# Kernel tuning notes

Hardware: AMD Instinct MI355X
Metric: run time of the kernel (lower is better)

## Reference

```python
import jax, jax.numpy as jnp
import numpy as np

NEG = -1e9
LRELU_ALPHA = 0.2  # tf.nn.leaky_relu default


def setup_inputs() -> dict:
    key = jax.random.key(0)
    k = jax.random.split(key, 6)
    B, N, F_in, F_out = 1, 8192, 256, 64
    x = jax.random.normal(k[0], (B, N, F_in), dtype=jnp.float32)
    # sparse adjacency as additive bias: ~32 neighbors/node on average
    u = jax.random.uniform(k[1], (B, N, N), dtype=jnp.float32)
    adj = jnp.where(u < 32.0 / N, 0.0, NEG).astype(jnp.float32)
    W = jax.random.normal(k[2], (F_in, F_out), dtype=jnp.float32) * (1.0 / np.sqrt(F_in))
    a1 = jax.random.normal(k[3], (F_out, 1), dtype=jnp.float32) * (1.0 / np.sqrt(F_out))
    a2 = jax.random.normal(k[4], (F_out, 1), dtype=jnp.float32) * (1.0 / np.sqrt(F_out))
    b1 = jnp.zeros((1,), dtype=jnp.float32)
    b2 = jnp.zeros((1,), dtype=jnp.float32)
    bias = jnp.zeros((F_out,), dtype=jnp.float32)
    return {"x": x, "adj": adj, "W": W, "a1": a1, "b1": b1, "a2": a2, "b2": b2, "bias": bias}


def reference(x, adj, W, a1, b1, a2, b2, bias):
    # conv1 (kernel_size=1, no bias) == per-node linear projection
    fts = jnp.einsum('bnf,fo->bno', x, W)            # [B, N, F_out]
    f1 = jnp.einsum('bno,oi->bni', fts, a1) + b1     # [B, N, 1]
    f2 = jnp.einsum('bno,oi->bni', fts, a2) + b2     # [B, N, 1]
    logits = f1 + jnp.swapaxes(f2, 1, 2)             # [B, N, N] additive scores
    scores = jax.nn.leaky_relu(logits, LRELU_ALPHA) + adj
    coefs = jax.nn.softmax(scores, axis=-1)          # [B, N, N]
    vals = jnp.einsum('bnm,bmo->bno', coefs, fts) + bias
    return jax.nn.elu(vals)
```

## Files before the change

kernel.cpp:

```cpp
#include <hip/hip_runtime.h>
#include <cstdint>

#define N_NODES 8192
#define F_IN    256
#define F_OUT   64
#define ALPHA   0.2f
#define CAPG    128

typedef float f32x4 __attribute__((ext_vector_type(4)));

__global__ __launch_bounds__(256) void k_proj(const float* __restrict__ x,
                                              const float* __restrict__ W,
                                              const float* __restrict__ a1,
                                              const float* __restrict__ b1,
                                              const float* __restrict__ a2,
                                              const float* __restrict__ b2,
                                              float* __restrict__ fts,
                                              float* __restrict__ f1,
                                              float* __restrict__ f2) {
    __shared__ __align__(16) float ws[64][F_OUT];
    const int t = threadIdx.x, lane = t & 63, w = t >> 6;
    const int rowA = blockIdx.x * 8 + w * 2;
    const int rowB = rowA + 1;

    const float4* xqA = (const float4*)(x + (size_t)rowA * F_IN);
    const float4* xqB = (const float4*)(x + (size_t)rowB * F_IN);
    float accA = 0.f, accB = 0.f;

    for (int kc = 0; kc < 4; ++kc) {
        if (kc) __syncthreads();
        {
            const float4* Wt = (const float4*)(W + (size_t)kc * 64 * F_OUT);
            float4* S = (float4*)&ws[0][0];
            S[t]       = Wt[t];
            S[t + 256] = Wt[t + 256];
            S[t + 512] = Wt[t + 512];
            S[t + 768] = Wt[t + 768];
        }
        __syncthreads();
        #pragma unroll
        for (int q = 0; q < 16; ++q) {
            const float4 xa = xqA[kc * 16 + q];
            const float4 xb = xqB[kc * 16 + q];
            const float w0 = ws[q*4+0][lane];
            const float w1 = ws[q*4+1][lane];
            const float w2 = ws[q*4+2][lane];
            const float w3 = ws[q*4+3][lane];
            accA += xa.x*w0 + xa.y*w1 + xa.z*w2 + xa.w*w3;
            accB += xb.x*w0 + xb.y*w1 + xb.z*w2 + xb.w*w3;
        }
    }
    fts[(size_t)rowA * F_OUT + lane] = accA;
    fts[(size_t)rowB * F_OUT + lane] = accB;

    const float u1 = a1[lane], u2 = a2[lane];
    float sA1 = accA * u1, sA2 = accA * u2;
    float sB1 = accB * u1, sB2 = accB * u2;
    #pragma unroll
    for (int off = 32; off >= 1; off >>= 1) {
        sA1 += __shfl_xor(sA1, off, 64);
        sA2 += __shfl_xor(sA2, off, 64);
        sB1 += __shfl_xor(sB1, off, 64);
        sB2 += __shfl_xor(sB2, off, 64);
    }
    if (lane == 0) {
        const float bb1 = b1[0], bb2 = b2[0];
        f1[rowA] = sA1 + bb1;  f2[rowA] = sA2 + bb2;
        f1[rowB] = sB1 + bb1;  f2[rowB] = sB2 + bb2;
    }
}

__global__ __launch_bounds__(256) void k_mega(const float* __restrict__ adj,
                                              const float* __restrict__ fts,
                                              const float* __restrict__ f1,
                                              const float* __restrict__ f2,
                                              const float* __restrict__ bias,
                                              float* __restrict__ out) {
    __shared__ int lj[4][CAPG];

    const int lane = threadIdx.x & 63, w = threadIdx.x >> 6;
    const int row  = blockIdx.x * 4 + w;
    const f32x4* Ar = (const f32x4*)(adj + (size_t)row * N_NODES);

    int cnt = 0;
    #pragma unroll 1
    for (int cb = 0; cb < 2048; cb += 256) {
        const f32x4 v0 = __builtin_nontemporal_load(&Ar[cb + lane]);
        const f32x4 v1 = __builtin_nontemporal_load(&Ar[cb + 64 + lane]);
        const f32x4 v2 = __builtin_nontemporal_load(&Ar[cb + 128 + lane]);
        const f32x4 v3 = __builtin_nontemporal_load(&Ar[cb + 192 + lane]);

        #define SCAN4(v, qb)                                                          \
        {                                                                             \
            unsigned long long mx = __ballot((v)[0] > -0.5f);                         \
            unsigned long long my = __ballot((v)[1] > -0.5f);                         \
            unsigned long long mz = __ballot((v)[2] > -0.5f);                         \
            unsigned long long mw = __ballot((v)[3] > -0.5f);                         \
            while (mx) { const int l = __ffsll((long long)mx) - 1; mx &= mx - 1;      \
                if (lane == 0 && cnt < CAPG) lj[w][cnt] = (((qb) + l) << 2) | 0;      \
                ++cnt; }                                                              \
            while (my) { const int l = __ffsll((long long)my) - 1; my &= my - 1;      \
                if (lane == 0 && cnt < CAPG) lj[w][cnt] = (((qb) + l) << 2) | 1;      \
                ++cnt; }                                                              \
            while (mz) { const int l = __ffsll((long long)mz) - 1; mz &= mz - 1;      \
                if (lane == 0 && cnt < CAPG) lj[w][cnt] = (((qb) + l) << 2) | 2;      \
                ++cnt; }                                                              \
            while (mw) { const int l = __ffsll((long long)mw) - 1; mw &= mw - 1;      \
                if (lane == 0 && cnt < CAPG) lj[w][cnt] = (((qb) + l) << 2) | 3;      \
                ++cnt; }                                                              \
        }
        SCAN4(v0, cb)
        SCAN4(v1, cb + 64)
        SCAN4(v2, cb + 128)
        SCAN4(v3, cb + 192)
        #undef SCAN4
    }

    const int n = (cnt < CAPG) ? cnt : CAPG;
    const float f1r = f1[row];

    float l0 = -3.0e38f, l1 = -3.0e38f;
    int   j0 = 0, j1 = 0;
    if (lane < n)      { j0 = lj[w][lane];      const float g = f1r + f2[j0]; l0 = fmaxf(g, ALPHA * g); }
    if (lane + 64 < n) { j1 = lj[w][lane + 64]; const float g = f1r + f2[j1]; l1 = fmaxf(g, ALPHA * g); }

    float m = fmaxf(l0, l1);
    #pragma unroll
    for (int off = 32; off >= 1; off >>= 1)
        m = fmaxf(m, __shfl_xor(m, off, 64));

    const float p0 = __expf(l0 - m);
    const float p1 = __expf(l1 - m);

    float den = p0 + p1;
    #pragma unroll
    for (int off = 32; off >= 1; off >>= 1)
        den += __shfl_xor(den, off, 64);

    float acc = 0.f;
    {
        const int nb = (n < 64) ? n : 64;
        for (int k = 0; k < nb; ++k)
            acc += __shfl(p0, k, 64) * fts[(size_t)__shfl(j0, k, 64) * F_OUT + lane];
    }
    if (n > 64) {
        const int nb = n - 64;
        for (int k = 0; k < nb; ++k)
            acc += __shfl(p1, k, 64) * fts[(size_t)__shfl(j1, k, 64) * F_OUT + lane];
    }

    const float v = acc / den + bias[lane];
    out[(size_t)row * F_OUT + lane] = (v > 0.f) ? v : expm1f(v);
}

extern "C" void kernel_launch(void* const* d_in, const int* in_sizes, int n_in,
                              void* d_out, int out_size, void* d_ws, size_t ws_size,
                              hipStream_t stream) {
    const float* x    = (const float*)d_in[0];
    const float* adj  = (const float*)d_in[1];
    const float* W    = (const float*)d_in[2];
    const float* a1   = (const float*)d_in[3];
    const float* b1   = (const float*)d_in[4];
    const float* a2   = (const float*)d_in[5];
    const float* b2   = (const float*)d_in[6];
    const float* bias = (const float*)d_in[7];
    float* out = (float*)d_out;

    float* fts = (float*)d_ws;
    float* f1  = fts + (size_t)N_NODES * F_OUT;
    float* f2  = f1 + N_NODES;

    k_proj<<<N_NODES / 8, 256, 0, stream>>>(x, W, a1, b1, a2, b2, fts, f1, f2);
    k_mega<<<N_NODES / 4, 256, 0, stream>>>(adj, fts, f1, f2, bias, out);
}
```

Measured before the change: 384.2 us.

## Replace serial ballot-based neighbor compaction with per-lane bitmasks and wave prefix scan

The adjacency scan used to ballot each component and have the whole wave walk every set bit serially, with lane 0 writing indices to LDS. Now each lane packs its 16 comparisons per chunk into a register bitmask, the wave computes per-lane offsets with a shuffle-based prefix sum, and each lane writes its own neighbor columns to LDS in parallel. This takes the serialized bit-walk loop off the critical path of the memory stream and lets loads be unrolled. The neighbor order changes (lane-major rather than column order), which only affects summation order, and the kernel now holds eight mask registers per lane.

```diff
diff --git a/kernel.cpp b/kernel.cpp
--- a/kernel.cpp
+++ b/kernel.cpp
@@ -82,41 +82,59 @@
     const int row  = blockIdx.x * 4 + w;
     const f32x4* Ar = (const f32x4*)(adj + (size_t)row * N_NODES);
 
-    int cnt = 0;
-    #pragma unroll 1
-    for (int cb = 0; cb < 2048; cb += 256) {
+    unsigned mreg[8];
+    #pragma unroll 2
+    for (int it = 0; it < 8; ++it) {
+        const int cb = it * 256;
         const f32x4 v0 = __builtin_nontemporal_load(&Ar[cb + lane]);
         const f32x4 v1 = __builtin_nontemporal_load(&Ar[cb + 64 + lane]);
         const f32x4 v2 = __builtin_nontemporal_load(&Ar[cb + 128 + lane]);
         const f32x4 v3 = __builtin_nontemporal_load(&Ar[cb + 192 + lane]);
-
-        #define SCAN4(v, qb)                                                          \
-        {                                                                             \
-            unsigned long long mx = __ballot((v)[0] > -0.5f);                         \
-            unsigned long long my = __ballot((v)[1] > -0.5f);                         \
-            unsigned long long mz = __ballot((v)[2] > -0.5f);                         \
-            unsigned long long mw = __ballot((v)[3] > -0.5f);                         \
-            while (mx) { const int l = __ffsll((long long)mx) - 1; mx &= mx - 1;      \
-                if (lane == 0 && cnt < CAPG) lj[w][cnt] = (((qb) + l) << 2) | 0;      \
-                ++cnt; }                                                              \
-            while (my) { const int l = __ffsll((long long)my) - 1; my &= my - 1;      \
-                if (lane == 0 && cnt < CAPG) lj[w][cnt] = (((qb) + l) << 2) | 1;      \
-                ++cnt; }                                                              \
-            while (mz) { const int l = __ffsll((long long)mz) - 1; mz &= mz - 1;      \
-                if (lane == 0 && cnt < CAPG) lj[w][cnt] = (((qb) + l) << 2) | 2;      \
-                ++cnt; }                                                              \
-            while (mw) { const int l = __ffsll((long long)mw) - 1; mw &= mw - 1;      \
-                if (lane == 0 && cnt < CAPG) lj[w][cnt] = (((qb) + l) << 2) | 3;      \
-                ++cnt; }                                                              \
-        }
-        SCAN4(v0, cb)
-        SCAN4(v1, cb + 64)
-        SCAN4(v2, cb + 128)
-        SCAN4(v3, cb + 192)
-        #undef SCAN4
+        unsigned mm = 0;
+        mm |= (v0[0] > -0.5f) ? 0x0001u : 0u;
+        mm |= (v0[1] > -0.5f) ? 0x0002u : 0u;
+        mm |= (v0[2] > -0.5f) ? 0x0004u : 0u;
+        mm |= (v0[3] > -0.5f) ? 0x0008u : 0u;
+        mm |= (v1[0] > -0.5f) ? 0x0010u : 0u;
+        mm |= (v1[1] > -0.5f) ? 0x0020u : 0u;
+        mm |= (v1[2] > -0.5f) ? 0x0040u : 0u;
+        mm |= (v1[3] > -0.5f) ? 0x0080u : 0u;
+        mm |= (v2[0] > -0.5f) ? 0x0100u : 0u;
+        mm |= (v2[1] > -0.5f) ? 0x0200u : 0u;
+        mm |= (v2[2] > -0.5f) ? 0x0400u : 0u;
+        mm |= (v2[3] > -0.5f) ? 0x0800u : 0u;
+        mm |= (v3[0] > -0.5f) ? 0x1000u : 0u;
+        mm |= (v3[1] > -0.5f) ? 0x2000u : 0u;
+        mm |= (v3[2] > -0.5f) ? 0x4000u : 0u;
+        mm |= (v3[3] > -0.5f) ? 0x8000u : 0u;
+        mreg[it] = mm;
     }
 
-    const int n = (cnt < CAPG) ? cnt : CAPG;
+    int c = 0;
+    #pragma unroll
+    for (int it = 0; it < 8; ++it) c += __popc(mreg[it]);
+
+    int inc = c;
+    #pragma unroll
+    for (int d = 1; d < 64; d <<= 1) {
+        const int tv = __shfl_up(inc, d, 64);
+        if (lane >= d) inc += tv;
+    }
+    int off = inc - c;
+    const int total = __shfl(inc, 63, 64);
+
+    #pragma unroll
+    for (int it = 0; it < 8; ++it) {
+        unsigned mm = mreg[it];
+        while (mm) {
+            const int b = __ffs(mm) - 1;
+            mm &= mm - 1;
+            const int col = it * 1024 + ((b >> 2) << 8) + (lane << 2) + (b & 3);
+            if (off < CAPG) lj[w][off] = col;
+            ++off;
+        }
+    }
+    const int n = (total < CAPG) ? total : CAPG;
     const float f1r = f1[row];
 
     float l0 = -3.0e38f, l1 = -3.0e38f;
@@ -126,16 +144,16 @@
 
     float m = fmaxf(l0, l1);
     #pragma unroll
-    for (int off = 32; off >= 1; off >>= 1)
-        m = fmaxf(m, __shfl_xor(m, off, 64));
+    for (int o = 32; o >= 1; o >>= 1)
+        m = fmaxf(m, __shfl_xor(m, o, 64));
 
     const float p0 = __expf(l0 - m);
     const float p1 = __expf(l1 - m);
 
     float den = p0 + p1;
     #pragma unroll
-    for (int off = 32; off >= 1; off >>= 1)
-        den += __shfl_xor(den, off, 64);
+    for (int o = 32; o >= 1; o >>= 1)
+        den += __shfl_xor(den, o, 64);
 
     float acc = 0.f;
     {
```

Measured after the change: 375.6 us. 2.3% less time.
